# Kernel tuning notes

Measured on AMD Instinct MI355X. Metric: run time of the kernel, lower is better.

Reference implementation:

```python
import jax, jax.numpy as jnp
import numpy as np

D_MODEL, N_HEADS, N_LEVELS, N_POINTS = 256, 8, 4, 4
SHAPES = [(64, 64), (32, 32), (16, 16), (8, 8)]  # (H, W) per level
BATCH = 4


def setup_inputs() -> dict:
    key = jax.random.key(0)
    ks = jax.random.split(key, 10)
    C = D_MODEL
    Lv = sum(h * w for h, w in SHAPES)
    Lq = Lv  # encoder self-attention: queries are the flattened multiscale tokens
    B = BATCH
    s = 0.02
    query = jax.random.normal(ks[0], (B, Lq, C), jnp.float32)
    input_flatten = jax.random.normal(ks[1], (B, Lv, C), jnp.float32)
    reference_points = jax.random.uniform(ks[2], (B, Lq, N_LEVELS, 2), jnp.float32)
    spatial_shapes = jnp.array(SHAPES, jnp.int32)
    sizes = np.array([h * w for h, w in SHAPES], np.int32)
    level_start_index = jnp.asarray(np.concatenate([[0], np.cumsum(sizes)[:-1]]).astype(np.int32))
    w_val = jax.random.normal(ks[3], (C, C), jnp.float32) * s
    b_val = jnp.zeros((C,), jnp.float32)
    w_off = jax.random.normal(ks[4], (C, N_HEADS * N_LEVELS * N_POINTS * 2), jnp.float32) * s
    b_off = jax.random.normal(ks[5], (N_HEADS * N_LEVELS * N_POINTS * 2,), jnp.float32) * 2.0
    w_attn = jax.random.normal(ks[6], (C, N_HEADS * N_LEVELS * N_POINTS), jnp.float32) * s
    b_attn = jnp.zeros((N_HEADS * N_LEVELS * N_POINTS,), jnp.float32)
    w_out = jax.random.normal(ks[7], (C, C), jnp.float32) * s
    b_out = jnp.zeros((C,), jnp.float32)
    return dict(query=query, reference_points=reference_points, input_flatten=input_flatten,
                spatial_shapes=spatial_shapes, level_start_index=level_start_index,
                w_val=w_val, b_val=b_val, w_off=w_off, b_off=b_off,
                w_attn=w_attn, b_attn=b_attn, w_out=w_out, b_out=b_out)


def _bilinear_sample(value_l, loc_l, Hl, Wl):
    """grid_sample(bilinear, padding_mode='zeros', align_corners=False) equivalent.
    value_l: [B, nH, Hl*Wl, d]; loc_l: [B, nH, Lq, nP, 2] normalized to [0,1]."""
    x = loc_l[..., 0] * Wl - 0.5
    y = loc_l[..., 1] * Hl - 0.5
    x0f = jnp.floor(x); y0f = jnp.floor(y)
    wx1 = x - x0f; wy1 = y - y0f
    x0 = x0f.astype(jnp.int32); y0 = y0f.astype(jnp.int32)
    B, nH, Lq, nP = x0.shape
    out = jnp.zeros(value_l.shape[:2] + (Lq, nP, value_l.shape[-1]), value_l.dtype)
    for dy, wy in ((0, 1.0 - wy1), (1, wy1)):
        for dx, wx in ((0, 1.0 - wx1), (1, wx1)):
            xi = x0 + dx; yi = y0 + dy
            valid = (xi >= 0) & (xi < Wl) & (yi >= 0) & (yi < Hl)
            idx = jnp.clip(yi, 0, Hl - 1) * Wl + jnp.clip(xi, 0, Wl - 1)  # [B,nH,Lq,nP]
            g = jnp.take_along_axis(value_l, idx.reshape(B, nH, Lq * nP, 1), axis=2)
            g = g.reshape(B, nH, Lq, nP, -1)
            out = out + (wy * wx * valid.astype(value_l.dtype))[..., None] * g
    return out  # [B, nH, Lq, nP, d]


def reference(query, reference_points, input_flatten, spatial_shapes, level_start_index,
              w_val, b_val, w_off, b_off, w_attn, b_attn, w_out, b_out):
    B, Lq, C = query.shape
    nH, nL, nP = N_HEADS, N_LEVELS, N_POINTS
    d = C // nH
    shapes = np.asarray(spatial_shapes)
    starts = np.asarray(level_start_index)

    value = (input_flatten @ w_val + b_val).reshape(B, -1, nH, d)
    off = (query @ w_off + b_off).reshape(B, Lq, nH, nL, nP, 2)
    attn = jax.nn.softmax((query @ w_attn + b_attn).reshape(B, Lq, nH, nL * nP), axis=-1)
    attn = attn.reshape(B, Lq, nH, nL, nP)

    # offset normalizer is (W, H) per level
    norm = jnp.asarray(shapes[:, ::-1].astype(np.float32))
    # sampling locations: [B, Lq, nH, nL, nP, 2]
    loc = reference_points[:, :, None, :, None, :] + off / norm[None, None, None, :, None, :]

    out = jnp.zeros((B, Lq, nH, d), query.dtype)
    for l in range(nL):
        Hl, Wl = int(shapes[l, 0]), int(shapes[l, 1])
        s0 = int(starts[l])
        value_l = value[:, s0:s0 + Hl * Wl].transpose(0, 2, 1, 3)      # [B,nH,HW,d]
        loc_l = loc[:, :, :, l].transpose(0, 2, 1, 3, 4)               # [B,nH,Lq,nP,2]
        samp = _bilinear_sample(value_l, loc_l, Hl, Wl)                # [B,nH,Lq,nP,d]
        out = out + jnp.einsum('bhqpd,bqhp->bqhd', samp, attn[:, :, :, l])
    out = out.reshape(B, Lq, C)
    return out @ w_out + b_out
```

## Files before the change

### kernel.cpp

```cpp
#include <hip/hip_runtime.h>
#include <hip/hip_fp16.h>
#include <math.h>

#define LQ 5440
#define LV 5440
#define BATCH_ 4
#define M_TOT (BATCH_ * LQ)

typedef _Float16 f16x8 __attribute__((ext_vector_type(8)));
typedef _Float16 f16x2t __attribute__((ext_vector_type(2)));
typedef float f32x4 __attribute__((ext_vector_type(4)));
typedef unsigned int uint_t;

__device__ __forceinline__ uint_t f2h2(float a, float b) {
  const unsigned short ua = __half_as_ushort(__float2half(a));
  const unsigned short ub = __half_as_ushort(__float2half(b));
  return (uint_t)ua | ((uint_t)ub << 16);
}
__device__ __forceinline__ uint_t pkrtz(float a, float b) {
  auto r = __builtin_amdgcn_cvt_pkrtz(a, b);
  uint_t u;
  __builtin_memcpy(&u, &r, 4);
  return u;
}
__device__ __forceinline__ float lo_f(uint_t u) {
  f16x2t h; __builtin_memcpy(&h, &u, 4); return (float)h[0];
}
__device__ __forceinline__ float hi_f(uint_t u) {
  f16x2t h; __builtin_memcpy(&h, &u, 4); return (float)h[1];
}

__global__ __launch_bounds__(256) void conv_weights(
    const float* __restrict__ w_off, const float* __restrict__ w_out,
    const float* __restrict__ w_val, const float* __restrict__ w_attn,
    unsigned short* __restrict__ Wcat, unsigned short* __restrict__ Wo,
    unsigned short* __restrict__ Wvt,
    unsigned short* __restrict__ guard_pre, unsigned short* __restrict__ guard_post)
{
  __shared__ float tbuf[64][65];
  const int tid = threadIdx.x;
  if (blockIdx.x == 0 && blockIdx.y == 0 && tid < 64) {
    guard_pre[tid] = 0;
    guard_post[tid] = 0;
  }
  const int k0 = blockIdx.x * 64;
  const int yy = blockIdx.y;
  const float* src; unsigned short* dst; int N; int ntile; int roff = 0;
  if (yy < 4)       { src = w_off;  dst = Wcat; N = 256; ntile = yy; }
  else if (yy < 8)  { src = w_out;  dst = Wo;   N = 256; ntile = yy - 4; }
  else if (yy < 12) { src = w_val;  dst = Wvt;  N = 256; ntile = yy - 8; }
  else              { src = w_attn; dst = Wcat; N = 128; ntile = yy - 12; roff = 256; }
  const int n0 = ntile * 64;
#pragma unroll
  for (int i = 0; i < 16; ++i) {
    const int r = (tid >> 6) + i * 4;
    const int c = tid & 63;
    tbuf[r][c] = src[(size_t)(k0 + r) * N + n0 + c];
  }
  __syncthreads();
#pragma unroll
  for (int i = 0; i < 16; ++i) {
    const int n = (tid >> 6) + i * 4;
    const int kk = tid & 63;
    dst[(size_t)(roff + n0 + n) * 256 + k0 + kk] =
        __half_as_ushort(__float2half(tbuf[kk][n]));
  }
}

__global__ __launch_bounds__(256) void gemm_front(
    const float* __restrict__ ifl, const float* __restrict__ query,
    const unsigned short* __restrict__ Wvt, const unsigned short* __restrict__ Wcat,
    const float* __restrict__ b_val, const float* __restrict__ b_off,
    const float* __restrict__ b_attn,
    unsigned short* __restrict__ valb, unsigned short* __restrict__ offb,
    unsigned short* __restrict__ logitb)
{
  const int P = blockIdx.x;
  const int X = P & 7;
  const int j = P >> 3;
  const int p = j % 5;
  const int rblk = X * 22 + j / 5;
  if (rblk >= M_TOT / 128) return;

  __shared__ unsigned short Sh[2][128 * 64];
  unsigned short* As = Sh[0];
  unsigned short* Bs = Sh[1];
  const int tid = threadIdx.x;
  const int w = tid >> 6, lane = tid & 63;
  const int wm = w >> 1, wn = w & 1;
  const int lr = lane & 15, lk = lane >> 4;
  const bool isval = p < 2;
  const float* Af = isval ? ifl : query;
  const unsigned short* Bt = isval ? Wvt : Wcat;
  const int n0 = (isval ? p : p - 2) * 128;
  const int m0 = rblk * 128;

  f32x4 acc[4][4] = {};

  for (int t = 0; t < 4; ++t) {
    const int ka = t * 64;
#pragma unroll
    for (int i = 0; i < 4; ++i) {
      const int rbase = i * 32 + w * 8;
      const int row = rbase + (lane >> 3);
      const int slot = lane & 7;
      const int gs = slot ^ (row & 7);
      const unsigned short* gp = Bt + (size_t)(n0 + row) * 256 + ka + gs * 8;
      __builtin_amdgcn_global_load_lds(
          (const __attribute__((address_space(1))) uint_t*)gp,
          (__attribute__((address_space(3))) uint_t*)(Bs + rbase * 64), 16, 0, 0);
    }
#pragma unroll
    for (int i = 0; i < 4; ++i) {
      const int rbase = i * 32 + w * 8;
      const int row = rbase + (lane >> 3);
      const int slot = lane & 7;
      const int gs = slot ^ (row & 7);
      const float* gp = Af + (size_t)(m0 + row) * 256 + ka + gs * 8;
      const float4 a0 = *(const float4*)gp;
      const float4 a1 = *(const float4*)(gp + 4);
      *(uint4*)&As[(size_t)row * 64 + slot * 8] =
          make_uint4(pkrtz(a0.x, a0.y), pkrtz(a0.z, a0.w),
                     pkrtz(a1.x, a1.y), pkrtz(a1.z, a1.w));
    }
    asm volatile("s_waitcnt vmcnt(0)" ::: "memory");
    __syncthreads();
#pragma unroll
    for (int kk = 0; kk < 2; ++kk) {
      f16x8 af[4], bfv[4];
#pragma unroll
      for (int m = 0; m < 4; ++m) {
        const int row = wm * 64 + m * 16 + lr;
        const int so = (kk * 4 + lk) ^ (row & 7);
        af[m] = *(const f16x8*)((const char*)As + row * 128 + so * 16);
      }
#pragma unroll
      for (int n = 0; n < 4; ++n) {
        const int row = wn * 64 + n * 16 + lr;
        const int so = (kk * 4 + lk) ^ (row & 7);
        bfv[n] = *(const f16x8*)((const char*)Bs + row * 128 + so * 16);
      }
#pragma unroll
      for (int m = 0; m < 4; ++m)
#pragma unroll
        for (int n = 0; n < 4; ++n)
          acc[m][n] = __builtin_amdgcn_mfma_f32_16x16x32_f16(af[m], bfv[n], acc[m][n], 0, 0, 0);
    }
    __syncthreads();
  }

  if (!isval) {
#pragma unroll
    for (int n = 0; n < 4; ++n) {
      const int col = n0 + wn * 64 + n * 16 + lr;
      const float bv = (col < 256) ? b_off[col] : b_attn[col - 256];
#pragma unroll
      for (int m = 0; m < 4; ++m) {
        const int rbase = m0 + wm * 64 + m * 16 + lk * 4;
#pragma unroll
        for (int j2 = 0; j2 < 4; ++j2) {
          const float v = acc[m][n][j2] + bv;
          const int row = rbase + j2;
          const unsigned short hv = __half_as_ushort(__float2half(v));
          if (col < 256) offb[(size_t)row * 256 + col] = hv;
          else           logitb[(size_t)row * 128 + (col - 256)] = hv;
        }
      }
    }
  } else {
    unsigned short* Sb = &Sh[0][0];
#pragma unroll
    for (int n = 0; n < 4; ++n) {
      const int lcol = wn * 64 + n * 16 + lr;
      const float bv = b_val[n0 + lcol];
#pragma unroll
      for (int m = 0; m < 4; ++m) {
        const int lrow = wm * 64 + m * 16 + lk * 4;
#pragma unroll
        for (int j2 = 0; j2 < 4; ++j2)
          Sb[(size_t)(lrow + j2) * 128 + lcol] =
              __half_as_ushort(__float2half(acc[m][n][j2] + bv));
      }
    }
    __syncthreads();
#pragma unroll
    for (int it = 0; it < 8; ++it) {
      const int idx = it * 256 + tid;
      const int r  = idx >> 4;
      const int c8 = idx & 15;
      const uint_t row_g = (uint_t)(m0 + r);
      const uint_t bb  = row_g / (uint_t)LV;
      const uint_t pos = row_g - bb * (uint_t)LV;
      const int colg = n0 + c8 * 8;
      const uint_t hh = (uint_t)colg >> 5;
      const uint_t chо = (uint_t)colg & 31u;
      unsigned short* dp = valb + (((size_t)(bb * 8u + hh) * LV + pos) << 5) + chо;
      *(uint4*)dp = *(const uint4*)&Sb[(size_t)r * 128 + c8 * 8];
    }
  }
}

__global__ __launch_bounds__(256) void gemm_out(
    const unsigned short* __restrict__ A,
    const unsigned short* __restrict__ Bt,
    const float* __restrict__ bias,
    float* __restrict__ C)
{
  const int P = blockIdx.x;
  const int X = P & 7;
  const int j = P >> 3;
  const int p = j % 2;
  const int rblk = X * 22 + j / 2;
  if (rblk >= M_TOT / 128) return;

  __shared__ unsigned short As[128 * 64];
  __shared__ unsigned short Bs[128 * 64];
  const int tid = threadIdx.x;
  const int w = tid >> 6, lane = tid & 63;
  const int wm = w >> 1, wn = w & 1;
  const int lr = lane & 15, lk = lane >> 4;
  const int m0 = rblk * 128, n0 = p * 128;

  f32x4 acc[4][4] = {};

  for (int t = 0; t < 4; ++t) {
    const int ka = t * 64;
#pragma unroll
    for (int i = 0; i < 4; ++i) {
      const int rbase = i * 32 + w * 8;
      const int row = rbase + (lane >> 3);
      const int slot = lane & 7;
      const int gs = slot ^ (row & 7);
      const unsigned short* gp = A + (size_t)(m0 + row) * 256 + ka + gs * 8;
      __builtin_amdgcn_global_load_lds(
          (const __attribute__((address_space(1))) uint_t*)gp,
          (__attribute__((address_space(3))) uint_t*)(As + rbase * 64), 16, 0, 0);
    }
#pragma unroll
    for (int i = 0; i < 4; ++i) {
      const int rbase = i * 32 + w * 8;
      const int row = rbase + (lane >> 3);
      const int slot = lane & 7;
      const int gs = slot ^ (row & 7);
      const unsigned short* gp = Bt + (size_t)(n0 + row) * 256 + ka + gs * 8;
      __builtin_amdgcn_global_load_lds(
          (const __attribute__((address_space(1))) uint_t*)gp,
          (__attribute__((address_space(3))) uint_t*)(Bs + rbase * 64), 16, 0, 0);
    }
    asm volatile("s_waitcnt vmcnt(0)" ::: "memory");
    __syncthreads();
#pragma unroll
    for (int kk = 0; kk < 2; ++kk) {
      f16x8 af[4], bfv[4];
#pragma unroll
      for (int m = 0; m < 4; ++m) {
        const int row = wm * 64 + m * 16 + lr;
        const int so = (kk * 4 + lk) ^ (row & 7);
        af[m] = *(const f16x8*)((const char*)As + row * 128 + so * 16);
      }
#pragma unroll
      for (int n = 0; n < 4; ++n) {
        const int row = wn * 64 + n * 16 + lr;
        const int so = (kk * 4 + lk) ^ (row & 7);
        bfv[n] = *(const f16x8*)((const char*)Bs + row * 128 + so * 16);
      }
#pragma unroll
      for (int m = 0; m < 4; ++m)
#pragma unroll
        for (int n = 0; n < 4; ++n)
          acc[m][n] = __builtin_amdgcn_mfma_f32_16x16x32_f16(af[m], bfv[n], acc[m][n], 0, 0, 0);
    }
    __syncthreads();
  }
#pragma unroll
  for (int n = 0; n < 4; ++n) {
    const int col = n0 + wn * 64 + n * 16 + lr;
    const float bv = bias[col];
#pragma unroll
    for (int m = 0; m < 4; ++m) {
      const int rbase = m0 + wm * 64 + m * 16 + lk * 4;
#pragma unroll
      for (int j2 = 0; j2 < 4; ++j2)
        C[(size_t)(rbase + j2) * 256 + col] = acc[m][n][j2] + bv;
    }
  }
}

__global__ __launch_bounds__(256) void msda_sample_v16(
    const unsigned short* __restrict__ off_buf,
    const unsigned short* __restrict__ logit_buf,
    const unsigned short* __restrict__ value,
    const float* __restrict__ ref_pts,
    const int*  __restrict__ sshapes, const int* __restrict__ lstart,
    unsigned short* __restrict__ samp)
{
  __shared__ uint_t wlds[32 * 68];
  const int tid = threadIdx.x;
  const int P  = blockIdx.x;
  const int L  = (((P & 7) >> 1) * 1360) + ((P & 1) * 680) + (P >> 3);
  const int q0 = L * 4;
  const int b  = L / (LQ / 4);
  const int qp1 = tid >> 5;

  if (tid < 128) {
    const int h  = (tid >> 2) & 7;
    const int l  = tid & 3;
    const int qg = q0 + qp1;
    const int Hl = sshapes[2 * l], Wl = sshapes[2 * l + 1];
    const int st = lstart[l];
    const float rx = ref_pts[(size_t)qg * 8 + l * 2 + 0];
    const float ry = ref_pts[(size_t)qg * 8 + l * 2 + 1];
    const float fx = rx * (float)Wl - 0.5f;
    const float fy = ry * (float)Hl - 0.5f;

    const uint4 og = *(const uint4*)(off_buf + (size_t)qg * 256 + h * 32 + l * 8);
    const float offv[8] = {lo_f(og.x), hi_f(og.x), lo_f(og.y), hi_f(og.y),
                           lo_f(og.z), hi_f(og.z), lo_f(og.w), hi_f(og.w)};

    const uint2 lgu = *(const uint2*)(logit_buf + (size_t)qg * 128 + h * 16 + l * 4);
    float lg[4];
    lg[0] = lo_f(lgu.x); lg[1] = hi_f(lgu.x);
    lg[2] = lo_f(lgu.y); lg[3] = hi_f(lgu.y);

    float mx = fmaxf(fmaxf(lg[0], lg[1]), fmaxf(lg[2], lg[3]));
    mx = fmaxf(mx, __shfl_xor(mx, 1));
    mx = fmaxf(mx, __shfl_xor(mx, 2));
    float ex[4]; float ssum = 0.f;
#pragma unroll
    for (int p = 0; p < 4; ++p) { ex[p] = __expf(lg[p] - mx); ssum += ex[p]; }
    ssum += __shfl_xor(ssum, 1);
    ssum += __shfl_xor(ssum, 2);
    const float inv = 1.f / ssum;

    uint_t* wrow = wlds + (size_t)(qp1 * 8 + h) * 68;

#pragma unroll
    for (int p = 0; p < 4; ++p) {
      const float x = fx + offv[p * 2 + 0];
      const float y = fy + offv[p * 2 + 1];
      const float aw = ex[p] * inv;
      const float xf = floorf(x), yf = floorf(y);
      const int x0i = (int)xf, y0i = (int)yf;
      const float wx1 = x - xf, wy1 = y - yf;
      const float wx0 = 1.f - wx1, wy0 = 1.f - wy1;
      const int x1i = x0i + 1, y1i = y0i + 1;
      const bool vx0 = (uint_t)x0i < (uint_t)Wl, vx1 = (uint_t)x1i < (uint_t)Wl;
      const bool vy0 = (uint_t)y0i < (uint_t)Hl, vy1 = (uint_t)y1i < (uint_t)Hl;
      const float awy0 = aw * wy0, awy1 = aw * wy1;
      const float w00 = (vy0 && vx0) ? awy0 * wx0 : 0.f;
      const float w01 = (vy0 && vx1) ? awy0 * wx1 : 0.f;
      const float w10 = (vy1 && vx0) ? awy1 * wx0 : 0.f;
      const float w11 = (vy1 && vx1) ? awy1 * wx1 : 0.f;
      const int yc0 = min(max(y0i, 0), Hl - 1);
      const int yc1 = min(max(y1i, 0), Hl - 1);
      const int xr  = (vx0 || vx1) ? max(x0i, -1) : 0;
      const int i00 = st + yc0 * Wl + xr;
      const int i10 = st + yc1 * Wl + xr;
      uint4 pk;
      pk.x = f2h2(w00, w01);
      pk.y = f2h2(w10, w11);
      pk.z = ((uint_t)i00 & 0xffffu) | (((uint_t)i10 & 0xffffu) << 16);
      pk.w = 0u;
      *(uint4*)(wrow + (l * 4 + p) * 4) = pk;
    }
  }
  __syncthreads();

  const int grp = tid >> 3;
  const int g   = tid & 7;
  const int q2  = grp >> 3;
  const int h2  = grp & 7;
  const int qg2 = q0 + q2;
  const uint_t* wrow = wlds + (size_t)grp * 68;
  const char* vB = (const char*)value
      + ((size_t)(b * 8 + h2) * LV) * 64 + (size_t)g * 16;
  const int side = g >> 2;
  float acc[8] = {};

#pragma unroll
  for (int pt = 0; pt < 16; ++pt) {
    const uint4 pk = *(const uint4*)(wrow + pt * 4);
    const float wA = side ? hi_f(pk.x) : lo_f(pk.x);
    const float wB = side ? hi_f(pk.y) : lo_f(pk.y);
    const int i0 = (int)(short)(pk.z & 0xffffu);
    const int i1 = (int)(short)(pk.z >> 16);
    const f16x8 g0 = *(const f16x8*)(vB + (ptrdiff_t)i0 * 64);
    const f16x8 g1 = *(const f16x8*)(vB + (ptrdiff_t)i1 * 64);
#pragma unroll
    for (int c = 0; c < 8; ++c) acc[c] = fmaf((float)g0[c], wA, acc[c]);
#pragma unroll
    for (int c = 0; c < 8; ++c) acc[c] = fmaf((float)g1[c], wB, acc[c]);
  }

#pragma unroll
  for (int c = 0; c < 8; ++c) acc[c] += __shfl_xor(acc[c], 4);

  if (g < 4) {
    const uint4 o = make_uint4(pkrtz(acc[0], acc[1]), pkrtz(acc[2], acc[3]),
                               pkrtz(acc[4], acc[5]), pkrtz(acc[6], acc[7]));
    *(uint4*)(samp + (size_t)qg2 * 256 + h2 * 32 + g * 8) = o;
  }
}

extern "C" void kernel_launch(void* const* d_in, const int* in_sizes, int n_in,
                              void* d_out, int out_size, void* d_ws, size_t ws_size,
                              hipStream_t stream) {
  const float* query         = (const float*)d_in[0];
  const float* ref_pts       = (const float*)d_in[1];
  const float* input_flatten = (const float*)d_in[2];
  const int*   sshapes       = (const int*)d_in[3];
  const int*   lstart        = (const int*)d_in[4];
  const float* w_val  = (const float*)d_in[5];
  const float* b_val  = (const float*)d_in[6];
  const float* w_off  = (const float*)d_in[7];
  const float* b_off  = (const float*)d_in[8];
  const float* w_attn = (const float*)d_in[9];
  const float* b_attn = (const float*)d_in[10];
  const float* w_out  = (const float*)d_in[11];
  const float* b_out  = (const float*)d_in[12];
  float* out = (float*)d_out;

  char* ws = (char*)d_ws;
  unsigned short* guard_pre  = (unsigned short*)(ws);
  unsigned short* valb   = (unsigned short*)(ws + 128);
  unsigned short* guard_post = (unsigned short*)(ws + 11141248);
  unsigned short* samp   = (unsigned short*)(ws + 11141376);
  unsigned short* offb   = (unsigned short*)(ws + 22282496);
  unsigned short* logitb = (unsigned short*)(ws + 33423616);
  unsigned short* Wcat   = (unsigned short*)(ws + 38994176);
  unsigned short* Wo     = (unsigned short*)(ws + 39190784);
  unsigned short* Wvt    = (unsigned short*)(ws + 39321856);

  dim3 blk(256);
  conv_weights<<<dim3(4, 14), blk, 0, stream>>>(
      w_off, w_out, w_val, w_attn, Wcat, Wo, Wvt, guard_pre, guard_post);
  gemm_front<<<dim3(880), blk, 0, stream>>>(
      input_flatten, query, Wvt, Wcat, b_val, b_off, b_attn, valb, offb, logitb);
  msda_sample_v16<<<dim3(M_TOT / 4), blk, 0, stream>>>(
      offb, logitb, valb, ref_pts, sshapes, lstart, samp);
  gemm_out<<<dim3(352), blk, 0, stream>>>(samp, Wo, b_out, out);
}
```

Measured before the change: 73.94 us.

## Fuse deformable sampling with output projection GEMM in one kernel

Merges the sampling kernel and the output-projection GEMM into a single kernel. Each block now handles 16 queries: it computes the sampling weights, gathers values into an LDS tile, then multiplies that tile by Wo with MFMA and writes the final fp32 output. This removes the intermediate samp buffer round-trip and one kernel launch. In exchange, Wo is now read straight from global memory without LDS staging and re-read by every one of the 1360 blocks. The larger LDS footprint per block may also reduce occupancy for the gather phase.

```diff
diff --git a/kernel.cpp b/kernel.cpp
--- a/kernel.cpp
+++ b/kernel.cpp
@@ -6,6 +6,7 @@
 #define LV 5440
 #define BATCH_ 4
 #define M_TOT (BATCH_ * LQ)
+#define QB 16
 
 typedef _Float16 f16x8 __attribute__((ext_vector_type(8)));
 typedef _Float16 f16x2t __attribute__((ext_vector_type(2)));
@@ -193,119 +194,38 @@
       const uint_t pos = row_g - bb * (uint_t)LV;
       const int colg = n0 + c8 * 8;
       const uint_t hh = (uint_t)colg >> 5;
-      const uint_t chо = (uint_t)colg & 31u;
-      unsigned short* dp = valb + (((size_t)(bb * 8u + hh) * LV + pos) << 5) + chо;
+      const uint_t ch = (uint_t)colg & 31u;
+      unsigned short* dp = valb + (((size_t)(bb * 8u + hh) * LV + pos) << 5) + ch;
       *(uint4*)dp = *(const uint4*)&Sb[(size_t)r * 128 + c8 * 8];
     }
   }
 }
 
-__global__ __launch_bounds__(256) void gemm_out(
-    const unsigned short* __restrict__ A,
-    const unsigned short* __restrict__ Bt,
-    const float* __restrict__ bias,
-    float* __restrict__ C)
-{
-  const int P = blockIdx.x;
-  const int X = P & 7;
-  const int j = P >> 3;
-  const int p = j % 2;
-  const int rblk = X * 22 + j / 2;
-  if (rblk >= M_TOT / 128) return;
-
-  __shared__ unsigned short As[128 * 64];
-  __shared__ unsigned short Bs[128 * 64];
-  const int tid = threadIdx.x;
-  const int w = tid >> 6, lane = tid & 63;
-  const int wm = w >> 1, wn = w & 1;
-  const int lr = lane & 15, lk = lane >> 4;
-  const int m0 = rblk * 128, n0 = p * 128;
-
-  f32x4 acc[4][4] = {};
-
-  for (int t = 0; t < 4; ++t) {
-    const int ka = t * 64;
-#pragma unroll
-    for (int i = 0; i < 4; ++i) {
-      const int rbase = i * 32 + w * 8;
-      const int row = rbase + (lane >> 3);
-      const int slot = lane & 7;
-      const int gs = slot ^ (row & 7);
-      const unsigned short* gp = A + (size_t)(m0 + row) * 256 + ka + gs * 8;
-      __builtin_amdgcn_global_load_lds(
-          (const __attribute__((address_space(1))) uint_t*)gp,
-          (__attribute__((address_space(3))) uint_t*)(As + rbase * 64), 16, 0, 0);
-    }
-#pragma unroll
-    for (int i = 0; i < 4; ++i) {
-      const int rbase = i * 32 + w * 8;
-      const int row = rbase + (lane >> 3);
-      const int slot = lane & 7;
-      const int gs = slot ^ (row & 7);
-      const unsigned short* gp = Bt + (size_t)(n0 + row) * 256 + ka + gs * 8;
-      __builtin_amdgcn_global_load_lds(
-          (const __attribute__((address_space(1))) uint_t*)gp,
-          (__attribute__((address_space(3))) uint_t*)(Bs + rbase * 64), 16, 0, 0);
-    }
-    asm volatile("s_waitcnt vmcnt(0)" ::: "memory");
-    __syncthreads();
-#pragma unroll
-    for (int kk = 0; kk < 2; ++kk) {
-      f16x8 af[4], bfv[4];
-#pragma unroll
-      for (int m = 0; m < 4; ++m) {
-        const int row = wm * 64 + m * 16 + lr;
-        const int so = (kk * 4 + lk) ^ (row & 7);
-        af[m] = *(const f16x8*)((const char*)As + row * 128 + so * 16);
-      }
-#pragma unroll
-      for (int n = 0; n < 4; ++n) {
-        const int row = wn * 64 + n * 16 + lr;
-        const int so = (kk * 4 + lk) ^ (row & 7);
-        bfv[n] = *(const f16x8*)((const char*)Bs + row * 128 + so * 16);
-      }
-#pragma unroll
-      for (int m = 0; m < 4; ++m)
-#pragma unroll
-        for (int n = 0; n < 4; ++n)
-          acc[m][n] = __builtin_amdgcn_mfma_f32_16x16x32_f16(af[m], bfv[n], acc[m][n], 0, 0, 0);
-    }
-    __syncthreads();
-  }
-#pragma unroll
-  for (int n = 0; n < 4; ++n) {
-    const int col = n0 + wn * 64 + n * 16 + lr;
-    const float bv = bias[col];
-#pragma unroll
-    for (int m = 0; m < 4; ++m) {
-      const int rbase = m0 + wm * 64 + m * 16 + lk * 4;
-#pragma unroll
-      for (int j2 = 0; j2 < 4; ++j2)
-        C[(size_t)(rbase + j2) * 256 + col] = acc[m][n][j2] + bv;
-    }
-  }
-}
-
-__global__ __launch_bounds__(256) void msda_sample_v16(
+__global__ __launch_bounds__(256) void msda_fused(
     const unsigned short* __restrict__ off_buf,
     const unsigned short* __restrict__ logit_buf,
     const unsigned short* __restrict__ value,
     const float* __restrict__ ref_pts,
     const int*  __restrict__ sshapes, const int* __restrict__ lstart,
-    unsigned short* __restrict__ samp)
+    const unsigned short* __restrict__ Wo,
+    const float* __restrict__ b_out,
+    float* __restrict__ out)
 {
-  __shared__ uint_t wlds[32 * 68];
+  __shared__ uint_t wlds[128 * 68];
+  __shared__ unsigned short samp_lds[QB][264];
   const int tid = threadIdx.x;
   const int P  = blockIdx.x;
-  const int L  = (((P & 7) >> 1) * 1360) + ((P & 1) * 680) + (P >> 3);
-  const int q0 = L * 4;
-  const int b  = L / (LQ / 4);
-  const int qp1 = tid >> 5;
-
-  if (tid < 128) {
-    const int h  = (tid >> 2) & 7;
-    const int l  = tid & 3;
-    const int qg = q0 + qp1;
+  const int L  = (((P & 7) >> 1) * 340) + ((P & 1) * 170) + (P >> 3);
+  const int q0 = L * QB;
+  const int b  = L / (LQ / QB);
+
+#pragma unroll
+  for (int i = 0; i < 2; ++i) {
+    const int task = tid + i * 256;
+    const int q  = task >> 5;
+    const int h  = (task >> 2) & 7;
+    const int l  = task & 3;
+    const int qg = q0 + q;
     const int Hl = sshapes[2 * l], Wl = sshapes[2 * l + 1];
     const int st = lstart[l];
     const float rx = ref_pts[(size_t)qg * 8 + l * 2 + 0];
@@ -327,18 +247,18 @@
     mx = fmaxf(mx, __shfl_xor(mx, 2));
     float ex[4]; float ssum = 0.f;
 #pragma unroll
-    for (int p = 0; p < 4; ++p) { ex[p] = __expf(lg[p] - mx); ssum += ex[p]; }
+    for (int pp = 0; pp < 4; ++pp) { ex[pp] = __expf(lg[pp] - mx); ssum += ex[pp]; }
     ssum += __shfl_xor(ssum, 1);
     ssum += __shfl_xor(ssum, 2);
     const float inv = 1.f / ssum;
 
-    uint_t* wrow = wlds + (size_t)(qp1 * 8 + h) * 68;
-
-#pragma unroll
-    for (int p = 0; p < 4; ++p) {
-      const float x = fx + offv[p * 2 + 0];
-      const float y = fy + offv[p * 2 + 1];
-      const float aw = ex[p] * inv;
+    uint_t* wrow = wlds + (size_t)(q * 8 + h) * 68;
+
+#pragma unroll
+    for (int pp = 0; pp < 4; ++pp) {
+      const float x = fx + offv[pp * 2 + 0];
+      const float y = fy + offv[pp * 2 + 1];
+      const float aw = ex[pp] * inv;
       const float xf = floorf(x), yf = floorf(y);
       const int x0i = (int)xf, y0i = (int)yf;
       const float wx1 = x - xf, wy1 = y - yf;
@@ -361,44 +281,73 @@
       pk.y = f2h2(w10, w11);
       pk.z = ((uint_t)i00 & 0xffffu) | (((uint_t)i10 & 0xffffu) << 16);
       pk.w = 0u;
-      *(uint4*)(wrow + (l * 4 + p) * 4) = pk;
+      *(uint4*)(wrow + (l * 4 + pp) * 4) = pk;
     }
   }
   __syncthreads();
 
-  const int grp = tid >> 3;
-  const int g   = tid & 7;
-  const int q2  = grp >> 3;
-  const int h2  = grp & 7;
-  const int qg2 = q0 + q2;
-  const uint_t* wrow = wlds + (size_t)grp * 68;
-  const char* vB = (const char*)value
-      + ((size_t)(b * 8 + h2) * LV) * 64 + (size_t)g * 16;
-  const int side = g >> 2;
-  float acc[8] = {};
-
-#pragma unroll
-  for (int pt = 0; pt < 16; ++pt) {
-    const uint4 pk = *(const uint4*)(wrow + pt * 4);
-    const float wA = side ? hi_f(pk.x) : lo_f(pk.x);
-    const float wB = side ? hi_f(pk.y) : lo_f(pk.y);
-    const int i0 = (int)(short)(pk.z & 0xffffu);
-    const int i1 = (int)(short)(pk.z >> 16);
-    const f16x8 g0 = *(const f16x8*)(vB + (ptrdiff_t)i0 * 64);
-    const f16x8 g1 = *(const f16x8*)(vB + (ptrdiff_t)i1 * 64);
-#pragma unroll
-    for (int c = 0; c < 8; ++c) acc[c] = fmaf((float)g0[c], wA, acc[c]);
-#pragma unroll
-    for (int c = 0; c < 8; ++c) acc[c] = fmaf((float)g1[c], wB, acc[c]);
-  }
-
-#pragma unroll
-  for (int c = 0; c < 8; ++c) acc[c] += __shfl_xor(acc[c], 4);
-
-  if (g < 4) {
-    const uint4 o = make_uint4(pkrtz(acc[0], acc[1]), pkrtz(acc[2], acc[3]),
-                               pkrtz(acc[4], acc[5]), pkrtz(acc[6], acc[7]));
-    *(uint4*)(samp + (size_t)qg2 * 256 + h2 * 32 + g * 8) = o;
+  {
+    const int g    = tid & 7;
+    const int side = g >> 2;
+#pragma unroll
+    for (int gi = 0; gi < 4; ++gi) {
+      const int grp = gi * 32 + (tid >> 3);
+      const int q2  = grp >> 3;
+      const int h2  = grp & 7;
+      const uint_t* wrow = wlds + (size_t)grp * 68;
+      const char* vB = (const char*)value
+          + ((size_t)(b * 8 + h2) * LV) * 64 + (size_t)g * 16;
+      float acc[8] = {};
+#pragma unroll
+      for (int pt = 0; pt < 16; ++pt) {
+        const uint4 pk = *(const uint4*)(wrow + pt * 4);
+        const float wA = side ? hi_f(pk.x) : lo_f(pk.x);
+        const float wB = side ? hi_f(pk.y) : lo_f(pk.y);
+        const int i0 = (int)(short)(pk.z & 0xffffu);
+        const int i1 = (int)(short)(pk.z >> 16);
+        const f16x8 g0 = *(const f16x8*)(vB + (ptrdiff_t)i0 * 64);
+        const f16x8 g1 = *(const f16x8*)(vB + (ptrdiff_t)i1 * 64);
+#pragma unroll
+        for (int c = 0; c < 8; ++c) acc[c] = fmaf((float)g0[c], wA, acc[c]);
+#pragma unroll
+        for (int c = 0; c < 8; ++c) acc[c] = fmaf((float)g1[c], wB, acc[c]);
+      }
+#pragma unroll
+      for (int c = 0; c < 8; ++c) acc[c] += __shfl_xor(acc[c], 4);
+      if (g < 4) {
+        const uint4 o = make_uint4(pkrtz(acc[0], acc[1]), pkrtz(acc[2], acc[3]),
+                                   pkrtz(acc[4], acc[5]), pkrtz(acc[6], acc[7]));
+        *(uint4*)&samp_lds[q2][h2 * 32 + g * 8] = o;
+      }
+    }
+  }
+  __syncthreads();
+
+  {
+    const int w  = tid >> 6;
+    const int lane = tid & 63;
+    const int lr = lane & 15, lk = lane >> 4;
+    f32x4 acc2[4] = {};
+#pragma unroll
+    for (int ks = 0; ks < 8; ++ks) {
+      const f16x8 af = *(const f16x8*)&samp_lds[lr][ks * 32 + lk * 8];
+#pragma unroll
+      for (int nt = 0; nt < 4; ++nt) {
+        const int col = w * 64 + nt * 16 + lr;
+        const f16x8 bf = *(const f16x8*)(Wo + (size_t)col * 256 + ks * 32 + lk * 8);
+        acc2[nt] = __builtin_amdgcn_mfma_f32_16x16x32_f16(af, bf, acc2[nt], 0, 0, 0);
+      }
+    }
+#pragma unroll
+    for (int nt = 0; nt < 4; ++nt) {
+      const int col = w * 64 + nt * 16 + lr;
+      const float bv = b_out[col];
+#pragma unroll
+      for (int j2 = 0; j2 < 4; ++j2) {
+        const int row = lk * 4 + j2;
+        out[(size_t)(q0 + row) * 256 + col] = acc2[nt][j2] + bv;
+      }
+    }
   }
 }
 
@@ -424,19 +373,17 @@
   unsigned short* guard_pre  = (unsigned short*)(ws);
   unsigned short* valb   = (unsigned short*)(ws + 128);
   unsigned short* guard_post = (unsigned short*)(ws + 11141248);
-  unsigned short* samp   = (unsigned short*)(ws + 11141376);
-  unsigned short* offb   = (unsigned short*)(ws + 22282496);
-  unsigned short* logitb = (unsigned short*)(ws + 33423616);
-  unsigned short* Wcat   = (unsigned short*)(ws + 38994176);
-  unsigned short* Wo     = (unsigned short*)(ws + 39190784);
-  unsigned short* Wvt    = (unsigned short*)(ws + 39321856);
+  unsigned short* offb   = (unsigned short*)(ws + 11141376);
+  unsigned short* logitb = (unsigned short*)(ws + 22282496);
+  unsigned short* Wcat   = (unsigned short*)(ws + 27853056);
+  unsigned short* Wo     = (unsigned short*)(ws + 28049664);
+  unsigned short* Wvt    = (unsigned short*)(ws + 28180736);
 
   dim3 blk(256);
   conv_weights<<<dim3(4, 14), blk, 0, stream>>>(
       w_off, w_out, w_val, w_attn, Wcat, Wo, Wvt, guard_pre, guard_post);
   gemm_front<<<dim3(880), blk, 0, stream>>>(
       input_flatten, query, Wvt, Wcat, b_val, b_off, b_attn, valb, offb, logitb);
-  msda_sample_v16<<<dim3(M_TOT / 4), blk, 0, stream>>>(
-      offb, logitb, valb, ref_pts, sshapes, lstart, samp);
-  gemm_out<<<dim3(352), blk, 0, stream>>>(samp, Wo, b_out, out);
-}
+  msda_fused<<<dim3(M_TOT / QB), blk, 0, stream>>>(
+      offb, logitb, valb, ref_pts, sshapes, lstart, Wo, b_out, out);
+}
```

Result: slower. 89.64 us (+21.2%).
